# Performance work log

Hardware: AMD Instinct MI355X
Metric: run time of the kernel (lower is better)

The kernel has to match this reference:

```python
import jax, jax.numpy as jnp
import numpy as np

D_MODEL = 768
N_HEADS = 12
D_HEAD = 64
WINDOW = 16
LOOK_BACK = 1
IGNORE = -1.0e6


def look_around(x, backward=LOOK_BACK, forward=0, pad_value=0):
    # x: (b, n_windows, w, ...) -> (b, n_windows, w*(backward+forward+1), ...)
    n = x.shape[1]
    pad = [(0, 0)] * x.ndim
    pad[1] = (backward, forward)
    px = jnp.pad(x, pad, constant_values=pad_value)
    return jnp.concatenate([px[:, i:i + n] for i in range(backward + forward + 1)], axis=2)


def setup_inputs() -> dict:
    key = jax.random.key(0)
    k1, k2, k3 = jax.random.split(key, 3)
    B, T = 2, 2048
    x = jax.random.normal(k1, (B, T, D_MODEL), dtype=jnp.float32)
    W_abcde = jax.random.normal(k2, (D_MODEL, 5 * N_HEADS * D_HEAD), dtype=jnp.float32) * (1.0 / np.sqrt(D_MODEL))
    b_abcde = jnp.zeros((5 * N_HEADS * D_HEAD,), dtype=jnp.float32)
    W_O = jax.random.normal(k3, (N_HEADS * D_HEAD, D_MODEL), dtype=jnp.float32) * (1.0 / np.sqrt(N_HEADS * D_HEAD))
    b_O = jnp.zeros((D_MODEL,), dtype=jnp.float32)
    return {"x": x, "W_abcde": W_abcde, "b_abcde": b_abcde, "W_O": W_O, "b_O": b_O}


def reference(x, W_abcde, b_abcde, W_O, b_O):
    B, T, _ = x.shape
    w = WINDOW
    nw = T // w
    Ww = w * (LOOK_BACK + 1)  # look-around window length

    abcde = x @ W_abcde + b_abcde                                    # (B,T,5*H*D)
    abcde = abcde.reshape(B, T, 5, N_HEADS, D_HEAD).transpose(2, 0, 3, 1, 4)  # (5,B,H,T,D)
    a, b, c, d, e = [t.reshape(B * N_HEADS, nw, w, D_HEAD) for t in abcde]
    a_l, b_l, d_l, e_l = (look_around(t) for t in (a, b, d, e))       # (BH,nw,Ww,D)

    # causal mask, same construction as get_causal_mask (pad_value=0)
    seq = jnp.arange(T).reshape(1, nw, w)
    bb = look_around(seq)                                            # (1,nw,Ww)
    # mask[n,m,l] = (seq_n < bb_l) | (bb_l <= bb_m)
    mask = (seq[..., :, None, None] < bb[..., None, None, :]) | (bb[..., None, None, :] <= bb[..., None, :, None])

    # third-order attention scores: (BH, nw, w, Ww, Ww)
    scores = jnp.einsum('bnwd,bnmd,bnld->bnwml', c, a_l, b_l)
    scores = jnp.where(mask, IGNORE, scores)
    scores = jnp.where(scores == 0, IGNORE, scores)
    probs = jax.nn.softmax((scores / D_HEAD).reshape(B * N_HEADS, nw, w, Ww * Ww), axis=-1)
    probs = probs.reshape(scores.shape)

    z = jnp.einsum('bnwml,bnmd->bnwd', probs, d_l) + jnp.einsum('bnwml,bnld->bnwd', probs, e_l)
    z = z.reshape(B, N_HEADS, nw, w, D_HEAD).transpose(0, 2, 3, 1, 4).reshape(B, T, N_HEADS * D_HEAD)
    return z @ W_O + b_O
```

## Files before the change

### kernel.cpp

```cpp
#include <hip/hip_runtime.h>

#define T_SEQ   2048
#define NHEADS  12
#define DHEAD   64
#define WIN     16
#define WW      32
#define NWIN    128
#define DMODEL  768
#define NABCDE  3840
#define IGNORE_V (-1.0e6f)
#define PAD_K   72
#define L2E64   0.022542110013890053f

typedef float f32x4 __attribute__((ext_vector_type(4)));
typedef short bf16x8 __attribute__((ext_vector_type(8)));

__device__ __forceinline__ short f2bf(float f) {
    unsigned u = __float_as_uint(f);
    unsigned r = (u + 0x7FFF + ((u >> 16) & 1)) >> 16;
    return (short)r;
}

__device__ __forceinline__ void gload_lds16(const short* g, short* l) {
    __builtin_amdgcn_global_load_lds(
        (const __attribute__((address_space(1))) void*)g,
        (__attribute__((address_space(3))) void*)l,
        16, 0, 0);
}

__global__ __launch_bounds__(256) void prep_kernel(
    const float* __restrict__ x, const float* __restrict__ W_abcde,
    const float* __restrict__ W_O,
    short* __restrict__ xb, short* __restrict__ Wt, short* __restrict__ WOt)
{
    __shared__ float tile[32][33];
    const int blk = blockIdx.x;
    const int tid = threadIdx.x;

    if (blk < 1536) {
        int i = (blk * 256 + tid) * 8;
        float4 a = *reinterpret_cast<const float4*>(&x[i]);
        float4 b = *reinterpret_cast<const float4*>(&x[i + 4]);
        union { short s[8]; uint4 u; } r;
        r.s[0] = f2bf(a.x); r.s[1] = f2bf(a.y); r.s[2] = f2bf(a.z); r.s[3] = f2bf(a.w);
        r.s[4] = f2bf(b.x); r.s[5] = f2bf(b.y); r.s[6] = f2bf(b.z); r.s[7] = f2bf(b.w);
        *reinterpret_cast<uint4*>(&xb[i]) = r.u;
        return;
    }
    const float* W; short* Wo; int N, bx, by;
    if (blk < 4416) {
        int t = blk - 1536;
        W = W_abcde; Wo = Wt; N = NABCDE;
        bx = (t % 120) * 32; by = (t / 120) * 32;
    } else {
        int t = blk - 4416;
        W = W_O; Wo = WOt; N = DMODEL;
        bx = (t % 24) * 32; by = (t / 24) * 32;
    }
    const int tx = tid & 31, ty = tid >> 5;
#pragma unroll
    for (int r = 0; r < 32; r += 8)
        tile[ty + r][tx] = W[(size_t)(by + ty + r) * N + bx + tx];
    __syncthreads();
#pragma unroll
    for (int r = 0; r < 32; r += 8)
        Wo[(size_t)(bx + ty + r) * DMODEL + by + tx] = f2bf(tile[tx][ty + r]);
}

template <bool BF16OUT>
__global__ __launch_bounds__(256) void gemm_bf16_n64(
    const short* __restrict__ A, const short* __restrict__ Bt,
    const float* __restrict__ bias, void* __restrict__ Cv,
    int M, int N, int K)
{
    __shared__ short As[2][128 * 32];
    __shared__ short Bs[2][64 * 32];

    const int tid  = threadIdx.x;
    const int wave = tid >> 6;
    const int lane = tid & 63;
    const int bm = blockIdx.y * 128;
    const int bn = blockIdx.x * 64;

    const int st_row = lane >> 2;
    const int st_col = (lane & 3) * 8;
    const int fr_m = lane & 15;
    const int fr_k = (lane >> 4) * 8;
    const int wm = wave * 32;

    const short* gsrc[6];
    short* ldst[6];
#pragma unroll
    for (int j = 0; j < 6; ++j) {
        int c = wave * 6 + j;
        if (c < 16) {
            int kt = c >> 3, rg = c & 7;
            gsrc[j] = A + (size_t)(bm + rg * 16 + st_row) * K + kt * 32 + st_col;
            ldst[j] = &As[kt][(rg * 16) * 32];
        } else {
            int cb = c - 16;
            int kt = cb >> 2, rg = cb & 3;
            gsrc[j] = Bt + (size_t)(bn + rg * 16 + st_row) * K + kt * 32 + st_col;
            ldst[j] = &Bs[kt][(rg * 16) * 32];
        }
    }

    f32x4 acc[2][4];
#pragma unroll
    for (int mi = 0; mi < 2; ++mi)
#pragma unroll
        for (int ni = 0; ni < 4; ++ni) acc[mi][ni] = (f32x4){0.f, 0.f, 0.f, 0.f};

    for (int k0 = 0; k0 < K; k0 += 64) {
#pragma unroll
        for (int j = 0; j < 6; ++j) gload_lds16(gsrc[j] + k0, ldst[j]);
        __syncthreads();

#pragma unroll
        for (int kt = 0; kt < 2; ++kt) {
            bf16x8 af[2], bf[4];
#pragma unroll
            for (int mi = 0; mi < 2; ++mi)
                af[mi] = *reinterpret_cast<const bf16x8*>(
                    &As[kt][(wm + mi * 16 + fr_m) * 32 + fr_k]);
#pragma unroll
            for (int ni = 0; ni < 4; ++ni)
                bf[ni] = *reinterpret_cast<const bf16x8*>(
                    &Bs[kt][(ni * 16 + fr_m) * 32 + fr_k]);
#pragma unroll
            for (int mi = 0; mi < 2; ++mi)
#pragma unroll
                for (int ni = 0; ni < 4; ++ni)
                    acc[mi][ni] = __builtin_amdgcn_mfma_f32_16x16x32_bf16(
                        af[mi], bf[ni], acc[mi][ni], 0, 0, 0);
        }
        __syncthreads();
    }

    float bv[4];
#pragma unroll
    for (int ni = 0; ni < 4; ++ni)
        bv[ni] = bias[bn + ni * 16 + (lane & 15)];
#pragma unroll
    for (int mi = 0; mi < 2; ++mi) {
        int rbase = bm + wm + mi * 16 + (lane >> 4) * 4;
#pragma unroll
        for (int r = 0; r < 4; ++r) {
            size_t off = (size_t)(rbase + r) * N + bn + (lane & 15);
#pragma unroll
            for (int ni = 0; ni < 4; ++ni) {
                float val = acc[mi][ni][r] + bv[ni];
                if (BF16OUT) ((short*)Cv)[off + ni * 16] = f2bf(val);
                else         ((float*)Cv)[off + ni * 16] = val;
            }
        }
    }
}

__global__ __launch_bounds__(256) void attn_kernel(
    const short* __restrict__ abcde, short* __restrict__ z)
{
    const int blk = blockIdx.x;
    const int n  = blk & (NWIN - 1);
    const int bh = blk >> 7;
    const int b  = bh / NHEADS;
    const int h  = bh % NHEADS;

    __shared__ short sc[WIN * PAD_K];
    __shared__ short sa[WW * PAD_K];
    __shared__ short sb[WW * PAD_K];
    __shared__ short sd[WW * PAD_K];
    __shared__ short se[WW * PAD_K];
    __shared__ short epA[WIN * PAD_K];
    __shared__ float sinv[WIN];

    const int tid = threadIdx.x;
    const size_t rowbase = ((size_t)b * T_SEQ) * NABCDE;
    const int hd = h * DHEAD;

    if (tid < 128) {
        int row = tid >> 3, ch = (tid & 7) * 8;
        *reinterpret_cast<uint4*>(&sc[row * PAD_K + ch]) =
            *reinterpret_cast<const uint4*>(
                &abcde[rowbase + (size_t)(n * WIN + row) * NABCDE + 2 * DMODEL + hd + ch]);
    }
    {
        int row = tid >> 3, ch = (tid & 7) * 8;
        int t = n * WIN - WIN + row;
        uint4 va = {0u, 0u, 0u, 0u}, vb = va, vd = va, ve = va;
        if (t >= 0) {
            size_t base = rowbase + (size_t)t * NABCDE + hd + ch;
            va = *reinterpret_cast<const uint4*>(&abcde[base + 0 * DMODEL]);
            vb = *reinterpret_cast<const uint4*>(&abcde[base + 1 * DMODEL]);
            vd = *reinterpret_cast<const uint4*>(&abcde[base + 3 * DMODEL]);
            ve = *reinterpret_cast<const uint4*>(&abcde[base + 4 * DMODEL]);
        }
        *reinterpret_cast<uint4*>(&sa[row * PAD_K + ch]) = va;
        *reinterpret_cast<uint4*>(&sb[row * PAD_K + ch]) = vb;
        *reinterpret_cast<uint4*>(&sd[row * PAD_K + ch]) = vd;
        *reinterpret_cast<uint4*>(&se[row * PAD_K + ch]) = ve;
    }
    __syncthreads();

    const int wv = tid >> 6;
    const int lane = tid & 63;
    const int lc = lane & 15;
    const int ko = lane >> 4;

    float cxl[2][4], cxh[2][4];
    bf16x8 bfrag[2][2];
#pragma unroll
    for (int kt = 0; kt < 2; ++kt) {
        union { bf16x8 v; unsigned u[4]; } Cf;
        Cf.v = *reinterpret_cast<const bf16x8*>(
            &sc[(wv * 4 + (lc & 3)) * PAD_K + kt * 32 + ko * 8]);
#pragma unroll
        for (int j = 0; j < 4; ++j) {
            cxl[kt][j] = __uint_as_float(Cf.u[j] << 16);
            cxh[kt][j] = __uint_as_float(Cf.u[j] & 0xffff0000u);
        }
        bfrag[0][kt] = *reinterpret_cast<const bf16x8*>(&sb[lc * PAD_K + kt * 32 + ko * 8]);
        bfrag[1][kt] = *reinterpret_cast<const bf16x8*>(&sb[(16 + lc) * PAD_K + kt * 32 + ko * 8]);
    }

    f32x4 acc[8][2];
#pragma unroll
    for (int mt = 0; mt < 8; ++mt) {
        acc[mt][0] = (f32x4){0.f, 0.f, 0.f, 0.f};
        acc[mt][1] = (f32x4){0.f, 0.f, 0.f, 0.f};
    }
#pragma unroll
    for (int mt = 0; mt < 8; ++mt) {
#pragma unroll
        for (int kt = 0; kt < 2; ++kt) {
            union { bf16x8 v; unsigned u[4]; } Ar, Rf;
            Ar.v = *reinterpret_cast<const bf16x8*>(
                &sa[(mt * 4 + (lc >> 2)) * PAD_K + kt * 32 + ko * 8]);
#pragma unroll
            for (int j = 0; j < 4; ++j) {
                float yl = __uint_as_float(Ar.u[j] << 16);
                float yh = __uint_as_float(Ar.u[j] & 0xffff0000u);
                unsigned pl = __float_as_uint(cxl[kt][j] * yl);
                unsigned ph = __float_as_uint(cxh[kt][j] * yh);
                Rf.u[j] = __builtin_amdgcn_perm(ph, pl, 0x07060302);
            }
            acc[mt][0] = __builtin_amdgcn_mfma_f32_16x16x32_bf16(Rf.v, bfrag[0][kt], acc[mt][0], 0, 0, 0);
            acc[mt][1] = __builtin_amdgcn_mfma_f32_16x16x32_bf16(Rf.v, bfrag[1][kt], acc[mt][1], 0, 0, 0);
        }
    }

    const int nbase = n * WIN;
    int bbl_h[2];
#pragma unroll
    for (int lt = 0; lt < 2; ++lt) {
        int l = lt * 16 + lc;
        bbl_h[lt] = (n == 0 && l < WIN) ? 0 : (nbase - WIN + l);
    }
    float mx[4] = {-3.4e38f, -3.4e38f, -3.4e38f, -3.4e38f};
#pragma unroll
    for (int mt = 0; mt < 8; ++mt) {
        int m = mt * 4 + ko;
        int bbm = (n == 0 && m < WIN) ? 0 : (nbase - WIN + m);
#pragma unroll
        for (int lt = 0; lt < 2; ++lt) {
            bool mgt = bbl_h[lt] > bbm;
#pragma unroll
            for (int reg = 0; reg < 4; ++reg) {
                int tq = nbase + wv * 4 + reg;
                float v = acc[mt][lt][reg];
                bool keep = (tq >= bbl_h[lt]) && mgt;
                if (!keep || v == 0.0f) v = IGNORE_V;
                acc[mt][lt][reg] = v;
                mx[reg] = fmaxf(mx[reg], v);
            }
        }
    }
#pragma unroll
    for (int reg = 0; reg < 4; ++reg) {
#pragma unroll
        for (int off = 1; off < 64; off <<= 1)
            mx[reg] = fmaxf(mx[reg], __shfl_xor(mx[reg], off, 64));
    }

    float c0[4];
#pragma unroll
    for (int reg = 0; reg < 4; ++reg) c0[reg] = -mx[reg] * L2E64;
#pragma unroll
    for (int mt = 0; mt < 8; ++mt)
#pragma unroll
        for (int lt = 0; lt < 2; ++lt)
#pragma unroll
            for (int reg = 0; reg < 4; ++reg)
                acc[mt][lt][reg] = exp2f(fmaf(acc[mt][lt][reg], L2E64, c0[reg]));

    float plv[2][4];
#pragma unroll
    for (int lt = 0; lt < 2; ++lt) {
#pragma unroll
        for (int reg = 0; reg < 4; ++reg) {
            float p = acc[0][lt][reg];
#pragma unroll
            for (int mt = 1; mt < 8; ++mt) p += acc[mt][lt][reg];
            p += __shfl_xor(p, 16, 64);
            p += __shfl_xor(p, 32, 64);
            plv[lt][reg] = p;
        }
        float w  = (ko & 1) ? plv[lt][1] : plv[lt][0];
        float w2 = (ko & 1) ? plv[lt][3] : plv[lt][2];
        float ww = (ko & 2) ? w2 : w;
        epA[(wv * 4 + ko) * PAD_K + 32 + lt * 16 + lc] = f2bf(ww);
    }

    {
        float s[4];
#pragma unroll
        for (int reg = 0; reg < 4; ++reg) {
            float t = plv[0][reg] + plv[1][reg];
            t += __shfl_xor(t, 1, 64);
            t += __shfl_xor(t, 2, 64);
            t += __shfl_xor(t, 4, 64);
            t += __shfl_xor(t, 8, 64);
            s[reg] = t;
        }
        if (lane == 0) {
#pragma unroll
            for (int reg = 0; reg < 4; ++reg) sinv[wv * 4 + reg] = 1.0f / s[reg];
        }
    }

    {
        float v8[8][4];
#pragma unroll
        for (int mt = 0; mt < 8; ++mt)
#pragma unroll
            for (int reg = 0; reg < 4; ++reg)
                v8[mt][reg] = acc[mt][0][reg] + acc[mt][1][reg];

        const bool s0 = lane & 1, s1 = lane & 2, s2 = lane & 4, s3 = lane & 8;
        float r1[4][4];
#pragma unroll
        for (int m2 = 0; m2 < 4; ++m2)
#pragma unroll
            for (int reg = 0; reg < 4; ++reg) {
                float u = v8[2 * m2][reg], w = v8[2 * m2 + 1][reg];
                float a = s0 ? w : u;
                float s = s0 ? u : w;
                r1[m2][reg] = a + __shfl_xor(s, 1, 64);
            }
        float r2[2][4];
#pragma unroll
        for (int m4 = 0; m4 < 2; ++m4)
#pragma unroll
            for (int reg = 0; reg < 4; ++reg) {
                float u = r1[2 * m4][reg], w = r1[2 * m4 + 1][reg];
                float a = s1 ? w : u;
                float s = s1 ? u : w;
                r2[m4][reg] = a + __shfl_xor(s, 2, 64);
            }
        float r3[4];
#pragma unroll
        for (int reg = 0; reg < 4; ++reg) {
            float u = r2[0][reg], w = r2[1][reg];
            float a = s2 ? w : u;
            float s = s2 ? u : w;
            r3[reg] = a + __shfl_xor(s, 4, 64);
        }
        float a0 = s3 ? r3[1] : r3[0];
        float q0 = s3 ? r3[0] : r3[1];
        float g0 = a0 + __shfl_xor(q0, 8, 64);
        float a1 = s3 ? r3[3] : r3[2];
        float q1 = s3 ? r3[2] : r3[3];
        float g1 = a1 + __shfl_xor(q1, 8, 64);

        int mcol = (lc & 7) * 4 + ko;
        int ib = wv * 4 + (lc >> 3);
        epA[ib * PAD_K + mcol]       = f2bf(g0);
        epA[(ib + 2) * PAD_K + mcol] = f2bf(g1);
    }

    const int dd = wv * 16 + lc;
    bf16x8 bd, be;
    {
        unsigned dv[8], ev[8];
#pragma unroll
        for (int j = 0; j < 8; ++j) {
            dv[j] = *reinterpret_cast<const unsigned short*>(&sd[(ko * 8 + j) * PAD_K + dd]);
            ev[j] = *reinterpret_cast<const unsigned short*>(&se[(ko * 8 + j) * PAD_K + dd]);
        }
        union { unsigned u[4]; bf16x8 v; } td, te;
#pragma unroll
        for (int j = 0; j < 4; ++j) {
            td.u[j] = __builtin_amdgcn_perm(dv[2 * j + 1], dv[2 * j], 0x05040100);
            te.u[j] = __builtin_amdgcn_perm(ev[2 * j + 1], ev[2 * j], 0x05040100);
        }
        bd = td.v; be = te.v;
    }
    __syncthreads();

    bf16x8 apm = *reinterpret_cast<const bf16x8*>(&epA[lc * PAD_K + ko * 8]);
    bf16x8 apl = *reinterpret_cast<const bf16x8*>(&epA[lc * PAD_K + 32 + ko * 8]);
    f32x4 zacc = (f32x4){0.f, 0.f, 0.f, 0.f};
    zacc = __builtin_amdgcn_mfma_f32_16x16x32_bf16(apm, bd, zacc, 0, 0, 0);
    zacc = __builtin_amdgcn_mfma_f32_16x16x32_bf16(apl, be, zacc, 0, 0, 0);

#pragma unroll
    for (int reg = 0; reg < 4; ++reg) {
        int i = ko * 4 + reg;
        z[((size_t)b * T_SEQ + nbase + i) * (NHEADS * DHEAD) + hd + dd] =
            f2bf(zacc[reg] * sinv[i]);
    }
}

extern "C" void kernel_launch(void* const* d_in, const int* in_sizes, int n_in,
                              void* d_out, int out_size, void* d_ws, size_t ws_size,
                              hipStream_t stream) {
    const float* x        = (const float*)d_in[0];
    const float* W_abcde  = (const float*)d_in[1];
    const float* b_abcde  = (const float*)d_in[2];
    const float* W_O      = (const float*)d_in[3];
    const float* b_O      = (const float*)d_in[4];
    float* out = (float*)d_out;

    char* ws = (char*)d_ws;
    short* abcde = (short*)ws;
    short* xb    = (short*)(ws + (size_t)31457280);
    short* Wt    = (short*)(ws + (size_t)31457280 + 6291456);
    short* WOt   = (short*)(ws + (size_t)31457280 + 6291456 + 5898240);
    short* zb    = xb;

    const int M = 2 * T_SEQ;

    prep_kernel<<<dim3(4992), dim3(256), 0, stream>>>(
        x, W_abcde, W_O, xb, Wt, WOt);

    gemm_bf16_n64<true><<<dim3(NABCDE / 64, M / 128), dim3(256), 0, stream>>>(
        xb, Wt, b_abcde, (void*)abcde, M, NABCDE, DMODEL);

    attn_kernel<<<dim3(2 * NHEADS * NWIN), dim3(256), 0, stream>>>(abcde, zb);

    gemm_bf16_n64<false><<<dim3(DMODEL / 64, M / 128), dim3(256), 0, stream>>>(
        zb, WOt, b_O, (void*)out, M, DMODEL, DMODEL);
}
```

Measured before the change: 180.8 us.

## Add 64x64 output GEMM, pack attention products as float2, raise attn occupancy

Adds a dedicated 64x64-tile bf16 GEMM for the output projection, which doubles the block count to 768 for better CU fill. The attention kernel's elementwise c*a products are rewritten as float2 vectors so the compiler can emit packed FP32 multiplies. A launch-bounds minimum of 6 blocks per CU is set on the attention kernel to raise occupancy. The risk is that the register cap causes spills, and that the smaller GEMM tile brings more loads per FLOP.

New measurement: 196.0 us. 8.4% more time.

```diff
diff --git a/kernel.cpp b/kernel.cpp
--- a/kernel.cpp
+++ b/kernel.cpp
@@ -13,6 +13,7 @@
 #define L2E64   0.022542110013890053f
 
 typedef float f32x4 __attribute__((ext_vector_type(4)));
+typedef float f32x2 __attribute__((ext_vector_type(2)));
 typedef short bf16x8 __attribute__((ext_vector_type(8)));
 
 __device__ __forceinline__ short f2bf(float f) {
@@ -157,7 +158,82 @@
     }
 }
 
-__global__ __launch_bounds__(256) void attn_kernel(
+__global__ __launch_bounds__(256) void gemm_bf16_64(
+    const short* __restrict__ A, const short* __restrict__ Bt,
+    const float* __restrict__ bias, float* __restrict__ C,
+    int M, int N, int K)
+{
+    __shared__ short As[2][64 * 32];
+    __shared__ short Bs[2][64 * 32];
+
+    const int tid  = threadIdx.x;
+    const int wave = tid >> 6;
+    const int lane = tid & 63;
+    const int bm = blockIdx.y * 64;
+    const int bn = blockIdx.x * 64;
+
+    const int st_row = lane >> 2;
+    const int st_col = (lane & 3) * 8;
+    const int fr_m = lane & 15;
+    const int fr_k = (lane >> 4) * 8;
+    const int wm = wave * 16;
+
+    const short* gsrc[4];
+    short* ldst[4];
+#pragma unroll
+    for (int j = 0; j < 4; ++j) {
+        int c = wave * 4 + j;
+        if (c < 8) {
+            int kt = c >> 2, rg = c & 3;
+            gsrc[j] = A + (size_t)(bm + rg * 16 + st_row) * K + kt * 32 + st_col;
+            ldst[j] = &As[kt][(rg * 16) * 32];
+        } else {
+            int cb = c - 8;
+            int kt = cb >> 2, rg = cb & 3;
+            gsrc[j] = Bt + (size_t)(bn + rg * 16 + st_row) * K + kt * 32 + st_col;
+            ldst[j] = &Bs[kt][(rg * 16) * 32];
+        }
+    }
+
+    f32x4 acc[4];
+#pragma unroll
+    for (int ni = 0; ni < 4; ++ni) acc[ni] = (f32x4){0.f, 0.f, 0.f, 0.f};
+
+    for (int k0 = 0; k0 < K; k0 += 64) {
+#pragma unroll
+        for (int j = 0; j < 4; ++j) gload_lds16(gsrc[j] + k0, ldst[j]);
+        __syncthreads();
+
+#pragma unroll
+        for (int kt = 0; kt < 2; ++kt) {
+            bf16x8 af = *reinterpret_cast<const bf16x8*>(
+                &As[kt][(wm + fr_m) * 32 + fr_k]);
+#pragma unroll
+            for (int ni = 0; ni < 4; ++ni) {
+                bf16x8 bf = *reinterpret_cast<const bf16x8*>(
+                    &Bs[kt][(ni * 16 + fr_m) * 32 + fr_k]);
+                acc[ni] = __builtin_amdgcn_mfma_f32_16x16x32_bf16(
+                    af, bf, acc[ni], 0, 0, 0);
+            }
+        }
+        __syncthreads();
+    }
+
+    float bv[4];
+#pragma unroll
+    for (int ni = 0; ni < 4; ++ni)
+        bv[ni] = bias[bn + ni * 16 + (lane & 15)];
+    int rbase = bm + wm + (lane >> 4) * 4;
+#pragma unroll
+    for (int r = 0; r < 4; ++r) {
+        size_t off = (size_t)(rbase + r) * N + bn + (lane & 15);
+#pragma unroll
+        for (int ni = 0; ni < 4; ++ni)
+            C[off + ni * 16] = acc[ni][r] + bv[ni];
+    }
+}
+
+__global__ __launch_bounds__(256, 6) void attn_kernel(
     const short* __restrict__ abcde, short* __restrict__ z)
 {
     const int blk = blockIdx.x;
@@ -207,7 +283,7 @@
     const int lc = lane & 15;
     const int ko = lane >> 4;
 
-    float cxl[2][4], cxh[2][4];
+    f32x2 c2[2][4];
     bf16x8 bfrag[2][2];
 #pragma unroll
     for (int kt = 0; kt < 2; ++kt) {
@@ -216,8 +292,8 @@
             &sc[(wv * 4 + (lc & 3)) * PAD_K + kt * 32 + ko * 8]);
 #pragma unroll
         for (int j = 0; j < 4; ++j) {
-            cxl[kt][j] = __uint_as_float(Cf.u[j] << 16);
-            cxh[kt][j] = __uint_as_float(Cf.u[j] & 0xffff0000u);
+            c2[kt][j] = (f32x2){__uint_as_float(Cf.u[j] << 16),
+                                __uint_as_float(Cf.u[j] & 0xffff0000u)};
         }
         bfrag[0][kt] = *reinterpret_cast<const bf16x8*>(&sb[lc * PAD_K + kt * 32 + ko * 8]);
         bfrag[1][kt] = *reinterpret_cast<const bf16x8*>(&sb[(16 + lc) * PAD_K + kt * 32 + ko * 8]);
@@ -238,11 +314,11 @@
                 &sa[(mt * 4 + (lc >> 2)) * PAD_K + kt * 32 + ko * 8]);
 #pragma unroll
             for (int j = 0; j < 4; ++j) {
-                float yl = __uint_as_float(Ar.u[j] << 16);
-                float yh = __uint_as_float(Ar.u[j] & 0xffff0000u);
-                unsigned pl = __float_as_uint(cxl[kt][j] * yl);
-                unsigned ph = __float_as_uint(cxh[kt][j] * yh);
-                Rf.u[j] = __builtin_amdgcn_perm(ph, pl, 0x07060302);
+                f32x2 y = (f32x2){__uint_as_float(Ar.u[j] << 16),
+                                  __uint_as_float(Ar.u[j] & 0xffff0000u)};
+                f32x2 p = c2[kt][j] * y;
+                Rf.u[j] = __builtin_amdgcn_perm(
+                    __float_as_uint(p[1]), __float_as_uint(p[0]), 0x07060302);
             }
             acc[mt][0] = __builtin_amdgcn_mfma_f32_16x16x32_bf16(Rf.v, bfrag[0][kt], acc[mt][0], 0, 0, 0);
             acc[mt][1] = __builtin_amdgcn_mfma_f32_16x16x32_bf16(Rf.v, bfrag[1][kt], acc[mt][1], 0, 0, 0);
@@ -438,6 +514,6 @@
 
     attn_kernel<<<dim3(2 * NHEADS * NWIN), dim3(256), 0, stream>>>(abcde, zb);
 
-    gemm_bf16_n64<false><<<dim3(DMODEL / 64, M / 128), dim3(256), 0, stream>>>(
-        zb, WOt, b_O, (void*)out, M, DMODEL, DMODEL);
-}
+    gemm_bf16_64<<<dim3(DMODEL / 64, M / 64), dim3(256), 0, stream>>>(
+        zb, WOt, b_O, out, M, DMODEL, DMODEL);
+}
```
